# Optimization experiments

Measured on AMD Instinct MI355X. Metric: run time of the kernel, lower is better.

The kernel has to match this reference:

```python
import jax, jax.numpy as jnp
import numpy as np

B, SQ, SKV = 8, 1, 8192
HIDDEN, NUM_HEADS, NUM_KV_HEADS, HEAD_DIM = 4096, 32, 8, 128


def _rotate_half(x):
    x1, x2 = jnp.split(x, 2, axis=-1)
    return jnp.concatenate([-x2, x1], axis=-1)


def setup_inputs() -> dict:
    key = jax.random.key(0)
    ks = jax.random.split(key, 9)
    f = jnp.float32
    return {
        "hidden_states": jax.random.normal(ks[0], (B, SQ, HIDDEN), f),
        "wq": jax.random.normal(ks[1], (HIDDEN, NUM_HEADS * HEAD_DIM), f) * 0.02,
        "wo": jax.random.normal(ks[2], (NUM_HEADS * HEAD_DIM, HIDDEN), f) * 0.02,
        "cos": jax.random.uniform(ks[3], (B, SQ, HEAD_DIM), f, -1.0, 1.0),
        "sin": jax.random.uniform(ks[4], (B, SQ, HEAD_DIM), f, -1.0, 1.0),
        "key_states": jax.random.normal(ks[5], (B, SQ, NUM_KV_HEADS, HEAD_DIM), f),
        "value_states": jax.random.normal(ks[6], (B, SQ, NUM_KV_HEADS, HEAD_DIM), f),
        "k_cache": jax.random.normal(ks[7], (B, SKV, NUM_KV_HEADS, HEAD_DIM), f),
        "v_cache": jax.random.normal(ks[8], (B, SKV, NUM_KV_HEADS, HEAD_DIM), f),
    }


def reference(hidden_states, wq, wo, cos, sin, key_states, value_states, k_cache, v_cache):
    b, sq, _ = hidden_states.shape
    d = cos.shape[-1]
    nkv = key_states.shape[2]
    nh = wq.shape[1] // d
    g = nh // nkv  # GQA group size

    # Q projection -> [b, sq, nh, d]
    q = (hidden_states @ wq).reshape(b, sq, nh, d)

    # inline RoPE on q and the new k (cos/sin broadcast over heads)
    c = cos[:, :, None, :]
    s = sin[:, :, None, :]
    q = q * c + _rotate_half(q) * s
    k_new = key_states * c + _rotate_half(key_states) * s

    # cache append
    K = jnp.concatenate([k_cache, k_new], axis=1)          # [b, skv+sq, nkv, d]
    V = jnp.concatenate([v_cache, value_states], axis=1)   # [b, skv+sq, nkv, d]

    # GQA attention without materializing repeated KV heads
    qr = q.reshape(b, sq, nkv, g, d)
    scale = d ** -0.5
    scores = jnp.einsum('bqngd,bknd->bngqk', qr, K) * scale  # [b,nkv,g,sq,skv+sq]
    probs = jax.nn.softmax(scores, axis=-1)
    out = jnp.einsum('bngqk,bknd->bqngd', probs, V).reshape(b, sq, nh * d)

    # O projection
    return out @ wo
```

## Files before the change

### kernel.cpp

```cpp
#include <hip/hip_runtime.h>

#define HIDDEN 4096
#define NH 32
#define NKV 8
#define HD 128
#define SKV 8192
#define S2 64
#define KPB 128
#define BUF 4
#define NT (KPB/BUF)
#define NPART 64
#define PSTRIDE 520
#define SCALE 0.08838834764831845f

__device__ __forceinline__ float4 ld4(const float* p){ return *(const float4*)p; }

__device__ __forceinline__ void gll16(const float* g, float* l){
    __builtin_amdgcn_global_load_lds(
        (const __attribute__((address_space(1))) unsigned int*)g,
        (__attribute__((address_space(3))) unsigned int*)l,
        16, 0, 0);
}

__global__ __launch_bounds__(256) void gemv_part(const float* __restrict__ vec,
                                                 const float* __restrict__ mat,
                                                 float* __restrict__ part)
{
    const int jb  = blockIdx.x;
    const int c   = blockIdx.y;
    const int tid = threadIdx.x;
    const int j0  = jb*1024 + tid*4;

    __shared__ float hid[64*8];
    {
        int t = tid;
        int b0 = t >> 6, i0 = t & 63;
        hid[i0*8 + b0] = vec[(size_t)b0*HIDDEN + c*64 + i0];
        t += 256;
        int b1 = t >> 6, i1 = t & 63;
        hid[i1*8 + b1] = vec[(size_t)b1*HIDDEN + c*64 + i1];
    }
    __syncthreads();

    float4 acc[8];
#pragma unroll
    for (int b=0;b<8;b++) acc[b] = make_float4(0.f,0.f,0.f,0.f);

    const float* mp = mat + (size_t)c*64*HIDDEN + j0;
#pragma unroll 8
    for (int ii=0; ii<64; ii++) {
        float4 w  = ld4(mp + (size_t)ii*HIDDEN);
        float4 h0 = *(const float4*)&hid[ii*8];
        float4 h1 = *(const float4*)&hid[ii*8+4];
        acc[0].x += h0.x*w.x; acc[0].y += h0.x*w.y; acc[0].z += h0.x*w.z; acc[0].w += h0.x*w.w;
        acc[1].x += h0.y*w.x; acc[1].y += h0.y*w.y; acc[1].z += h0.y*w.z; acc[1].w += h0.y*w.w;
        acc[2].x += h0.z*w.x; acc[2].y += h0.z*w.y; acc[2].z += h0.z*w.z; acc[2].w += h0.z*w.w;
        acc[3].x += h0.w*w.x; acc[3].y += h0.w*w.y; acc[3].z += h0.w*w.z; acc[3].w += h0.w*w.w;
        acc[4].x += h1.x*w.x; acc[4].y += h1.x*w.y; acc[4].z += h1.x*w.z; acc[4].w += h1.x*w.w;
        acc[5].x += h1.y*w.x; acc[5].y += h1.y*w.y; acc[5].z += h1.y*w.z; acc[5].w += h1.y*w.w;
        acc[6].x += h1.z*w.x; acc[6].y += h1.z*w.y; acc[6].z += h1.z*w.z; acc[6].w += h1.z*w.w;
        acc[7].x += h1.w*w.x; acc[7].y += h1.w*w.y; acc[7].z += h1.w*w.z; acc[7].w += h1.w*w.w;
    }
#pragma unroll
    for (int b=0;b<8;b++)
        *(float4*)(part + ((size_t)(c*8+b))*HIDDEN + j0) = acc[b];
}

__global__ __launch_bounds__(256) void q_reduce_rope(const float* __restrict__ part,
                                                     const float* __restrict__ cosb,
                                                     const float* __restrict__ sinb,
                                                     float* __restrict__ q_rope)
{
    const int b    = blockIdx.x >> 5;
    const int jseg = blockIdx.x & 31;
    const int tid  = threadIdx.x;
    const int jl   = tid & 127;
    const int cg   = tid >> 7;

    float a = 0.f;
    const float* pp = part + (size_t)(cg*32*8 + b)*HIDDEN + jseg*128 + jl;
#pragma unroll 8
    for (int c=0;c<32;c++) a += pp[(size_t)c*8*HIDDEN];

    __shared__ float lds[256];
    __shared__ float sum[128];
    lds[tid] = a;
    __syncthreads();
    if (tid < 128) sum[tid] = lds[tid] + lds[tid+128];
    __syncthreads();
    if (tid < 128) {
        const int d = tid;
        float x = sum[d];
        float p = sum[d ^ 64];
        float cv = cosb[b*HD + d], sv = sinb[b*HD + d];
        float r = (d < 64) ? (x*cv - p*sv) : (x*cv + p*sv);
        q_rope[(size_t)b*HIDDEN + jseg*128 + d] = r;
    }
}

__global__ __launch_bounds__(512) void attn_split(const float* __restrict__ qr,
                                                  const float* __restrict__ kc,
                                                  const float* __restrict__ vc,
                                                  float* __restrict__ part)
{
    const int split = blockIdx.x;
    const int b     = blockIdx.y;
    const int tid   = threadIdx.x;
    const int wave  = tid >> 6;
    const int lane  = tid & 63;
    const int kg    = lane >> 4;
    const int dl    = lane & 15;

    __shared__ __align__(16) float bufK[2][BUF*1024];
    __shared__ __align__(16) float bufV[2][BUF*1024];

    float4 q1[4], q2[4];
    const float* qb = qr + ((size_t)b*NH + wave*4)*HD;
#pragma unroll
    for (int h=0;h<4;h++){
        float4 x = ld4(qb + h*HD + dl*4);
        float4 y = ld4(qb + h*HD + 64 + dl*4);
        q1[h] = make_float4(x.x*SCALE, x.y*SCALE, x.z*SCALE, x.w*SCALE);
        q2[h] = make_float4(y.x*SCALE, y.y*SCALE, y.z*SCALE, y.w*SCALE);
    }

    float l[4] = {0.f,0.f,0.f,0.f};
    float4 acc1[4], acc2[4];
#pragma unroll
    for (int h=0;h<4;h++){
        acc1[h] = make_float4(0.f,0.f,0.f,0.f);
        acc2[h] = make_float4(0.f,0.f,0.f,0.f);
    }

    const float* kbase = kc + ((size_t)b*SKV + (size_t)split*KPB)*(NKV*HD);
    const float* vbase = vc + ((size_t)b*SKV + (size_t)split*KPB)*(NKV*HD);

    const int woff = wave*256 + lane*4;

    {
        const float* gk = kbase;
        const float* gv = vbase;
        gll16(gk + woff,        &bufK[0][wave*256]);
        gll16(gk + 2048 + woff, &bufK[0][2048 + wave*256]);
        gll16(gv + woff,        &bufV[0][wave*256]);
        gll16(gv + 2048 + woff, &bufV[0][2048 + wave*256]);
    }
    __syncthreads();

    int cur = 0;
    for (int t = 0; t < NT; ++t) {
        if (t + 1 < NT) {
            const float* gk = kbase + (size_t)(t+1)*(BUF*1024);
            const float* gv = vbase + (size_t)(t+1)*(BUF*1024);
            const int nb = cur ^ 1;
            gll16(gk + woff,        &bufK[nb][wave*256]);
            gll16(gk + 2048 + woff, &bufK[nb][2048 + wave*256]);
            gll16(gv + woff,        &bufV[nb][wave*256]);
            gll16(gv + 2048 + woff, &bufV[nb][2048 + wave*256]);
        }

        {
            const float* Kb = &bufK[cur][kg*1024 + wave*128];
            const float* Vb = &bufV[cur][kg*1024 + wave*128];
            float4 k1 = ld4(Kb + dl*4);
            float4 k2 = ld4(Kb + 64 + dl*4);
            float4 v1 = ld4(Vb + dl*4);
            float4 v2 = ld4(Vb + 64 + dl*4);
            float p[4];
#pragma unroll
            for (int h=0;h<4;h++){
                float sp = q1[h].x*k1.x + q1[h].y*k1.y + q1[h].z*k1.z + q1[h].w*k1.w
                         + q2[h].x*k2.x + q2[h].y*k2.y + q2[h].z*k2.z + q2[h].w*k2.w;
                sp += __shfl_xor(sp, 1);
                sp += __shfl_xor(sp, 2);
                sp += __shfl_xor(sp, 4);
                sp += __shfl_xor(sp, 8);
                p[h] = __expf(sp);
                l[h] += p[h];
            }
#pragma unroll
            for (int h=0;h<4;h++){
                float ph = p[h];
                acc1[h].x += ph*v1.x; acc1[h].y += ph*v1.y;
                acc1[h].z += ph*v1.z; acc1[h].w += ph*v1.w;
                acc2[h].x += ph*v2.x; acc2[h].y += ph*v2.y;
                acc2[h].z += ph*v2.z; acc2[h].w += ph*v2.w;
            }
        }

        __syncthreads();
        cur ^= 1;
    }

#pragma unroll
    for (int h=0;h<4;h++){
        float t;
        t = l[h];      t += __shfl_xor(t,16); t += __shfl_xor(t,32); l[h] = t;
        t = acc1[h].x; t += __shfl_xor(t,16); t += __shfl_xor(t,32); acc1[h].x = t;
        t = acc1[h].y; t += __shfl_xor(t,16); t += __shfl_xor(t,32); acc1[h].y = t;
        t = acc1[h].z; t += __shfl_xor(t,16); t += __shfl_xor(t,32); acc1[h].z = t;
        t = acc1[h].w; t += __shfl_xor(t,16); t += __shfl_xor(t,32); acc1[h].w = t;
        t = acc2[h].x; t += __shfl_xor(t,16); t += __shfl_xor(t,32); acc2[h].x = t;
        t = acc2[h].y; t += __shfl_xor(t,16); t += __shfl_xor(t,32); acc2[h].y = t;
        t = acc2[h].z; t += __shfl_xor(t,16); t += __shfl_xor(t,32); acc2[h].z = t;
        t = acc2[h].w; t += __shfl_xor(t,16); t += __shfl_xor(t,32); acc2[h].w = t;
    }

    float* pb = part + ((size_t)((b*NKV + wave)*S2 + split))*PSTRIDE;
    if (lane == 0){
#pragma unroll
        for (int h=0;h<4;h++) pb[h] = l[h];
    }
    if (kg == 0){
#pragma unroll
        for (int h=0;h<4;h++){
            *(float4*)(pb + 8 + h*HD + dl*4)      = acc1[h];
            *(float4*)(pb + 8 + h*HD + 64 + dl*4) = acc2[h];
        }
    }
}

__global__ __launch_bounds__(256) void attn_combine(const float* __restrict__ part,
                                                    const float* __restrict__ qr,
                                                    const float* __restrict__ knew,
                                                    const float* __restrict__ vnew,
                                                    const float* __restrict__ cosb,
                                                    const float* __restrict__ sinb,
                                                    float* __restrict__ attn_out)
{
    const int bn  = blockIdx.x;
    const int b   = bn >> 3;
    const int n   = bn & 7;
    const int tid = threadIdx.x;
    const int wave = tid >> 6;
    const int lane = tid & 63;
    const float* pp = part + (size_t)bn*NPART*PSTRIDE;

    __shared__ float sm[4];
    __shared__ float lds_l[NPART*4];

    lds_l[tid] = pp[(size_t)(tid>>2)*PSTRIDE + (tid&3)];

    {
        const float* kn = knew + (size_t)bn*HD;
        const float* cb = cosb + (size_t)b*HD;
        const float* sb = sinb + (size_t)b*HD;
        const float* qh = qr + ((size_t)b*NH + n*4 + wave)*HD;
        float k_lo = kn[lane], k_hi = kn[lane+64];
        float kr1 = k_lo*cb[lane]    - k_hi*sb[lane];
        float kr2 = k_hi*cb[lane+64] + k_lo*sb[lane+64];
        float sp = (qh[lane]*kr1 + qh[lane+64]*kr2) * SCALE;
        sp += __shfl_xor(sp, 1);
        sp += __shfl_xor(sp, 2);
        sp += __shfl_xor(sp, 4);
        sp += __shfl_xor(sp, 8);
        sp += __shfl_xor(sp, 16);
        sp += __shfl_xor(sp, 32);
        if (lane == 0) sm[wave] = __expf(sp);
    }
    __syncthreads();

    const int o = tid*2;
    const int h = o >> 7;
    const int d = o & 127;
    const float wn = sm[h];
    float L = wn;
#pragma unroll 8
    for (int p=0; p<NPART; p++) L += lds_l[p*4+h];

    const float* vn = vnew + (size_t)bn*HD;
    float a0 = wn * vn[d];
    float a1 = wn * vn[d+1];
    const float* ap = pp + 8 + h*HD + d;
#pragma unroll 8
    for (int p=0; p<NPART; p++){
        float2 v = *(const float2*)(ap + (size_t)p*PSTRIDE);
        a0 += v.x; a1 += v.y;
    }
    const float inv = 1.f / L;
    float* op = attn_out + ((size_t)b*NH + n*4 + h)*HD + d;
    op[0] = a0*inv; op[1] = a1*inv;
}

__global__ __launch_bounds__(256) void o_reduce(const float* __restrict__ part,
                                                float* __restrict__ out)
{
    const int b    = blockIdx.x >> 5;
    const int jseg = blockIdx.x & 31;
    const int tid  = threadIdx.x;
    const int jl   = tid & 127;
    const int cg   = tid >> 7;

    float a = 0.f;
    const float* pp = part + (size_t)(cg*32*8 + b)*HIDDEN + jseg*128 + jl;
#pragma unroll 8
    for (int c=0;c<32;c++) a += pp[(size_t)c*8*HIDDEN];

    __shared__ float lds[256];
    lds[tid] = a;
    __syncthreads();
    if (tid < 128)
        out[(size_t)b*HIDDEN + jseg*128 + tid] = lds[tid] + lds[tid+128];
}

extern "C" void kernel_launch(void* const* d_in, const int* in_sizes, int n_in,
                              void* d_out, int out_size, void* d_ws, size_t ws_size,
                              hipStream_t stream) {
    const float* hidden = (const float*)d_in[0];
    const float* wq     = (const float*)d_in[1];
    const float* wo     = (const float*)d_in[2];
    const float* cosb   = (const float*)d_in[3];
    const float* sinb   = (const float*)d_in[4];
    const float* knew   = (const float*)d_in[5];
    const float* vnew   = (const float*)d_in[6];
    const float* kc     = (const float*)d_in[7];
    const float* vc     = (const float*)d_in[8];
    float* out = (float*)d_out;

    float* ws        = (float*)d_ws;
    float* part      = ws;
    float* q_rope    = ws + 2097152;
    float* attn_out  = q_rope + 32768;
    float* attn_part = attn_out + 32768;

    gemv_part<<<dim3(4,64), 256, 0, stream>>>(hidden, wq, part);
    q_reduce_rope<<<256, 256, 0, stream>>>(part, cosb, sinb, q_rope);
    attn_split<<<dim3(S2, 8), 512, 0, stream>>>(q_rope, kc, vc, attn_part);
    attn_combine<<<64, 256, 0, stream>>>(attn_part, q_rope, knew, vnew, cosb, sinb, attn_out);
    gemv_part<<<dim3(4,64), 256, 0, stream>>>(attn_out, wo, part);
    o_reduce<<<256, 256, 0, stream>>>(part, out);
}
```

Before: 631.5 us.

## Triple-buffer KV loads with explicit vmcnt waits and halve attention splits

Replaces the double-buffered KV staging in the split attention kernel with a three-stage ring. Loads are issued two tiles ahead, and a single barrier per iteration is gated by explicit s_waitcnt vmcnt counts instead of two __syncthreads. It also halves the number of KV splits (each block now processes 256 keys), which halves the partial results the combine kernel must reduce. The trade is fewer blocks in flight (8x32 = 256 blocks), which may leave part of the GPU idle, plus more LDS per block.

```diff
diff --git a/kernel.cpp b/kernel.cpp
--- a/kernel.cpp
+++ b/kernel.cpp
@@ -5,11 +5,11 @@
 #define NKV 8
 #define HD 128
 #define SKV 8192
-#define S2 64
-#define KPB 128
+#define S2 32
+#define KPB 256
 #define BUF 4
 #define NT (KPB/BUF)
-#define NPART 64
+#define NPART 32
 #define PSTRIDE 520
 #define SCALE 0.08838834764831845f
 
@@ -111,8 +111,8 @@
     const int kg    = lane >> 4;
     const int dl    = lane & 15;
 
-    __shared__ __align__(16) float bufK[2][BUF*1024];
-    __shared__ __align__(16) float bufV[2][BUF*1024];
+    __shared__ __align__(16) float bufK[3][BUF*1024];
+    __shared__ __align__(16) float bufV[3][BUF*1024];
 
     float4 q1[4], q2[4];
     const float* qb = qr + ((size_t)b*NH + wave*4)*HD;
@@ -137,26 +137,29 @@
 
     const int woff = wave*256 + lane*4;
 
-    {
-        const float* gk = kbase;
-        const float* gv = vbase;
-        gll16(gk + woff,        &bufK[0][wave*256]);
-        gll16(gk + 2048 + woff, &bufK[0][2048 + wave*256]);
-        gll16(gv + woff,        &bufV[0][wave*256]);
-        gll16(gv + 2048 + woff, &bufV[0][2048 + wave*256]);
-    }
-    __syncthreads();
+#define STAGE(t_, s_) do { \
+        const float* gk = kbase + (size_t)(t_)*(BUF*1024); \
+        const float* gv = vbase + (size_t)(t_)*(BUF*1024); \
+        gll16(gk + woff,        &bufK[s_][wave*256]);        \
+        gll16(gk + 2048 + woff, &bufK[s_][2048 + wave*256]); \
+        gll16(gv + woff,        &bufV[s_][wave*256]);        \
+        gll16(gv + 2048 + woff, &bufV[s_][2048 + wave*256]); \
+    } while (0)
+
+    STAGE(0, 0);
+    STAGE(1, 1);
 
     int cur = 0;
     for (int t = 0; t < NT; ++t) {
-        if (t + 1 < NT) {
-            const float* gk = kbase + (size_t)(t+1)*(BUF*1024);
-            const float* gv = vbase + (size_t)(t+1)*(BUF*1024);
-            const int nb = cur ^ 1;
-            gll16(gk + woff,        &bufK[nb][wave*256]);
-            gll16(gk + 2048 + woff, &bufK[nb][2048 + wave*256]);
-            gll16(gv + woff,        &bufV[nb][wave*256]);
-            gll16(gv + 2048 + woff, &bufV[nb][2048 + wave*256]);
+        if (t == NT-1) asm volatile("s_waitcnt vmcnt(0)" ::: "memory");
+        else           asm volatile("s_waitcnt vmcnt(4)" ::: "memory");
+        __builtin_amdgcn_s_barrier();
+        asm volatile("" ::: "memory");
+        __builtin_amdgcn_sched_barrier(0);
+
+        if (t + 2 < NT) {
+            int s2 = cur + 2; if (s2 >= 3) s2 -= 3;
+            STAGE(t+2, s2);
         }
 
         {
@@ -188,9 +191,9 @@
             }
         }
 
-        __syncthreads();
-        cur ^= 1;
-    }
+        cur = (cur == 2) ? 0 : cur + 1;
+    }
+#undef STAGE
 
 #pragma unroll
     for (int h=0;h<4;h++){
@@ -239,7 +242,8 @@
     __shared__ float sm[4];
     __shared__ float lds_l[NPART*4];
 
-    lds_l[tid] = pp[(size_t)(tid>>2)*PSTRIDE + (tid&3)];
+    if (tid < NPART*4)
+        lds_l[tid] = pp[(size_t)(tid>>2)*PSTRIDE + (tid&3)];
 
     {
         const float* kn = knew + (size_t)bn*HD;
```

Measured after the change: 648.5 us. +2.7%, slower.
